# Kernel tuning notes

Measured on AMD Instinct MI355X. Metric: run time of the kernel, lower is better.

The kernel has to match this reference:

```python
import jax, jax.numpy as jnp
import numpy as np

B, D_DATA, D_DICT0, N_SAE, D_DICT = 2048, 768, 128, 128, 32


def _kaiming_uniform(key, shape, fan_in):
    # torch.nn.init.kaiming_uniform_ default: bound = sqrt(6 / fan_in) / sqrt(5-gain stuff) ~ use gain=sqrt(2)? match torch default a=sqrt(5) not needed; plain kaiming_uniform_ uses gain=sqrt(2): bound = sqrt(6/fan_in)*? Keep simple: bound = sqrt(6.0/fan_in)
    bound = np.sqrt(6.0 / fan_in)
    return jax.random.uniform(key, shape, jnp.float32, -bound, bound)


def setup_inputs() -> dict:
    key = jax.random.key(0)
    ks = jax.random.split(key, 6)
    x = jax.random.normal(ks[0], (B, D_DATA), jnp.float32)
    # top-level SAE params
    W_enc0 = _kaiming_uniform(ks[1], (D_DATA, D_DICT0), D_DATA)
    b_enc0 = jnp.zeros((D_DICT0,), jnp.float32)
    W_dec0 = _kaiming_uniform(ks[2], (D_DICT0, D_DATA), D_DICT0)
    W_dec0 = W_dec0 / jnp.linalg.norm(W_dec0, axis=-1, keepdims=True)
    b_dec0 = jnp.zeros((D_DATA,), jnp.float32)
    # sublayer (hierarchical) per-expert params
    W_enc1 = _kaiming_uniform(ks[3], (N_SAE, D_DATA, D_DICT), D_DATA)
    b_enc1 = jnp.zeros((N_SAE, D_DICT), jnp.float32)
    W_dec1 = _kaiming_uniform(ks[4], (N_SAE, D_DICT, D_DATA), D_DICT)
    W_dec1 = W_dec1 / jnp.linalg.norm(W_dec1, axis=-1, keepdims=True)
    b_dec1 = jnp.zeros((N_SAE, D_DATA), jnp.float32)
    return {"x": x, "W_enc0": W_enc0, "b_enc0": b_enc0, "W_dec0": W_dec0,
            "b_dec0": b_dec0, "W_enc1": W_enc1, "b_enc1": b_enc1,
            "W_dec1": W_dec1, "b_dec1": b_dec1}


def reference(x, W_enc0, b_enc0, W_dec0, b_dec0, W_enc1, b_enc1, W_dec1, b_dec1):
    # ---- sae_0 (standard SAE; scale/unscale are identity) ----
    acts0 = jax.nn.relu((x - b_dec0) @ W_enc0 + b_enc0)        # [B, D_DICT0]
    x0 = acts0 @ W_dec0 + b_dec0                               # [B, D_DATA]
    # ---- binary gate over experts (n_sae == d_dict0) ----
    gate = (acts0 > 0).astype(x.dtype)                         # [B, N_SAE]
    # ---- sublayer: gather-encode-decode-scatter, expressed densely with a
    # binary mask (gate only selects membership; gate value is not multiplied).
    # Avoid materializing [B, N_SAE, D_DATA] by distributing (x - b_dec1[j]):
    pre = (jnp.einsum('bd,jdk->bjk', x, W_enc1)
           - jnp.einsum('jd,jdk->jk', b_dec1, W_enc1)[None]
           + b_enc1[None])                                     # [B, N_SAE, D_DICT]
    acts1 = jax.nn.relu(pre) * gate[:, :, None]                # zero out ungated
    # scatter_add over experts: sum_j gated (acts1[b,j] @ W_dec1[j] + b_dec1[j])
    dec = jnp.einsum('bjk,jkd->bd', acts1, W_dec1) + gate @ b_dec1  # [B, D_DATA]
    return x0 + dec
```

## Files before the change

### kernel.cpp

```cpp
#include <hip/hip_runtime.h>
#include <hip/hip_bf16.h>
#include <stdint.h>

#define B_SZ   2048
#define DDATA  768
#define NSAE   128
#define NJK    4096
#define KA2    4352
#define SPLITK 4
#define KC2    1088

typedef unsigned short u16;
typedef short bf16x8 __attribute__((ext_vector_type(8)));
typedef float f32x4  __attribute__((ext_vector_type(4)));

static __device__ __forceinline__ u16 f2bf(float f) {
  __hip_bfloat16 h = __float2bfloat16(f);
  return *reinterpret_cast<u16*>(&h);
}

static __device__ __forceinline__ void gload16(const u16* g, u16* l) {
  __builtin_amdgcn_global_load_lds(
      (const __attribute__((address_space(1))) unsigned int*)g,
      (__attribute__((address_space(3))) unsigned int*)l,
      16, 0, 0);
}

__global__ __launch_bounds__(256) void k_front(const float* __restrict__ x,
                                               const float* __restrict__ We0,
                                               const float* __restrict__ be0,
                                               const float* __restrict__ bd0,
                                               const float* __restrict__ We1,
                                               const float* __restrict__ bd1,
                                               const float* __restrict__ be1,
                                               const float* __restrict__ Wd1,
                                               const float* __restrict__ Wd0,
                                               u16* __restrict__ W1T,
                                               float* __restrict__ cvp,
                                               u16* __restrict__ B2T,
                                               u16* __restrict__ xb,
                                               u16* __restrict__ A2) {
  __shared__ float smem[6280];
  const int bid = blockIdx.x, t = threadIdx.x;
  if (bid < 512) {
    const int b0 = bid * 4;
    float* xs   = smem;
    float* part = smem + 3072;
    float* wqp  = smem + 5120;
    float* xns  = smem + 5632;
#pragma unroll
    for (int i = 0; i < 3; ++i) {
      int idx = t + i * 256;
      int r = idx / 192, c4 = idx % 192;
      size_t go = (size_t)(b0 + r) * DDATA + c4 * 4;
      float4 v = *(const float4*)&x[go];
      ushort4 o;
      o.x = f2bf(v.x); o.y = f2bf(v.y); o.z = f2bf(v.z); o.w = f2bf(v.w);
      *(ushort4*)&xb[go] = o;
      float4 b4 = *(const float4*)&bd0[c4 * 4];
      v.x -= b4.x; v.y -= b4.y; v.z -= b4.z; v.w -= b4.w;
      *(float4*)&xs[r * DDATA + c4 * 4] = v;
    }
    __syncthreads();
    const int ln = t & 63, w = t >> 6;
    {
      float a = 0.f;
#pragma unroll
      for (int q = 0; q < 12; ++q) { float xv = xs[w * DDATA + ln + q * 64]; a += xv * xv; }
#pragma unroll
      for (int sh = 32; sh; sh >>= 1) a += __shfl_xor(a, sh, 64);
      if (ln == 0) xns[w] = a;
    }
    const int j0 = ln * 2;
    float a00=0.f,a01=0.f,a10=0.f,a11=0.f,a20=0.f,a21=0.f,a30=0.f,a31=0.f;
    float wq0=0.f, wq1=0.f;
    const int dbase = w * 192;
    for (int d = dbase; d < dbase + 192; d += 4) {
      float4 xv0 = *(const float4*)&xs[0 * DDATA + d];
      float4 xv1 = *(const float4*)&xs[1 * DDATA + d];
      float4 xv2 = *(const float4*)&xs[2 * DDATA + d];
      float4 xv3 = *(const float4*)&xs[3 * DDATA + d];
#pragma unroll
      for (int dd = 0; dd < 4; ++dd) {
        float2 w2 = *(const float2*)&We0[(size_t)(d + dd) * 128 + j0];
        float x0 = ((const float*)&xv0)[dd], x1 = ((const float*)&xv1)[dd];
        float x2 = ((const float*)&xv2)[dd], x3 = ((const float*)&xv3)[dd];
        a00 += x0 * w2.x; a01 += x0 * w2.y;
        a10 += x1 * w2.x; a11 += x1 * w2.y;
        a20 += x2 * w2.x; a21 += x2 * w2.y;
        a30 += x3 * w2.x; a31 += x3 * w2.y;
        wq0 += w2.x * w2.x; wq1 += w2.y * w2.y;
      }
    }
    *(float2*)&part[(w * 4 + 0) * 128 + j0] = make_float2(a00, a01);
    *(float2*)&part[(w * 4 + 1) * 128 + j0] = make_float2(a10, a11);
    *(float2*)&part[(w * 4 + 2) * 128 + j0] = make_float2(a20, a21);
    *(float2*)&part[(w * 4 + 3) * 128 + j0] = make_float2(a30, a31);
    *(float2*)&wqp[w * 128 + j0] = make_float2(wq0, wq1);
    __syncthreads();
    float p0 = be0[j0], p1 = be0[j0 + 1];
    float wn0 = 0.f, wn1 = 0.f;
#pragma unroll
    for (int q = 0; q < 4; ++q) {
      float2 pr = *(const float2*)&part[(q * 4 + w) * 128 + j0];
      p0 += pr.x; p1 += pr.y;
      float2 wr2 = *(const float2*)&wqp[q * 128 + j0];
      wn0 += wr2.x; wn1 += wr2.y;
    }
    const float sx = sqrtf(xns[w]);
    const float tau0 = 1e-4f * sx * sqrtf(wn0);
    const float tau1 = 1e-4f * sx * sqrtf(wn1);
    const int bb = b0 + w;
    const size_t row = (size_t)bb * KA2;
    unsigned pk = (unsigned)f2bf(p0 > 0.f ? p0 : 0.f) |
                  ((unsigned)f2bf(p1 > 0.f ? p1 : 0.f) << 16);
    unsigned gk = (p0 > 0.f ? 0x3F80u : 0u) | (p1 > 0.f ? 0x3F800000u : 0u);
    *(unsigned*)&A2[row + NJK + j0]       = pk;
    *(unsigned*)&A2[row + NJK + 128 + j0] = gk;
#pragma unroll
    for (int c = 0; c < 2; ++c) {
      float pv = c ? p1 : p0;
      float tv = c ? tau1 : tau0;
      unsigned long long mask = __ballot(fabsf(pv) <= tv);
      while (mask) {
        int src = (int)__builtin_ctzll(mask);
        mask &= mask - 1;
        int jj = src * 2 + c;
        double acc = 0.0;
#pragma unroll
        for (int q = 0; q < 12; ++q) {
          int d = ln + q * 64;
          acc += (double)(x[(size_t)bb * DDATA + d] - bd0[d]) *
                 (double)We0[(size_t)d * 128 + jj];
        }
#pragma unroll
        for (int sh = 32; sh; sh >>= 1) acc += __shfl_xor(acc, sh, 64);
        if (ln == src) {
          double pd = acc + (double)be0[jj];
          A2[row + NJK + jj]       = f2bf(pd > 0.0 ? (float)pd : 0.f);
          A2[row + NJK + 128 + jj] = (pd > 0.0) ? (u16)0x3F80 : (u16)0;
        }
      }
    }
  } else if (bid < 896) {
    const int e = bid - 512;
    const int j = e & 127, seg = e >> 7;
    float* ts  = smem;
    float* bds = smem + 64 * 33;
    float* red = smem + 64 * 33 + 64;
    const int k = t & 31, g = t >> 5;
    float cacc = 0.f;
    for (int db = seg * 4; db < seg * 4 + 4; ++db) {
      const float* src = We1 + (size_t)j * 24576 + db * 2048;
#pragma unroll
      for (int i = 0; i < 8; ++i) {
        int ee = t + i * 256;
        ts[(ee >> 5) * 33 + (ee & 31)] = src[ee];
      }
      if (t < 64) bds[t] = bd1[(size_t)j * DDATA + db * 64 + t];
      __syncthreads();
#pragma unroll
      for (int i = 0; i < 8; ++i) {
        int ee = t + i * 256;
        int kk = ee >> 6, d = ee & 63;
        W1T[(size_t)(j * 32 + kk) * DDATA + db * 64 + d] = f2bf(ts[d * 33 + kk]);
      }
#pragma unroll
      for (int q = 0; q < 8; ++q) {
        int d = g + 8 * q;
        cacc += ts[d * 33 + k] * bds[d];
      }
      __syncthreads();
    }
    red[g * 32 + k] = cacc;
    __syncthreads();
    if (g == 0) {
      float s = 0.f;
#pragma unroll
      for (int q = 0; q < 8; ++q) s += red[q * 32 + k];
      cvp[seg * 4096 + j * 32 + k] = (seg == 0 ? be1[j * 32 + k] : 0.f) - s;
    }
  } else {
    const int e2 = bid - 896;
    const int rb = e2 / 12, dbk = e2 % 12;
    const float* src; int r0, base;
    if (rb < 64)      { src = Wd1; r0 = rb * 64;        base = 0;    }
    else if (rb < 66) { src = Wd0; r0 = (rb - 64) * 64; base = 4096; }
    else              { src = bd1; r0 = (rb - 66) * 64; base = 4224; }
    const int d0 = dbk * 64;
#pragma unroll
    for (int i = 0; i < 16; ++i) {
      int ee = t + i * 256;
      int ri = ee >> 6, di = ee & 63;
      smem[ri * 65 + di] = src[(size_t)(r0 + ri) * DDATA + d0 + di];
    }
    __syncthreads();
#pragma unroll
    for (int i = 0; i < 16; ++i) {
      int ee = t + i * 256;
      int di = ee >> 6, ri = ee & 63;
      B2T[(size_t)(d0 + di) * KA2 + base + r0 + ri] = f2bf(smem[ri * 65 + di]);
    }
  }
}

template<int BM, int BN, int EPI>
__global__ __launch_bounds__(256) void k_gemm(const u16* __restrict__ A,
                                              const u16* __restrict__ Bm,
                                              int K, int Kc,
                                              float* __restrict__ outF,
                                              u16* __restrict__ A2,
                                              const float* __restrict__ cvec) {
  constexpr int WM = BM / 32, WN = BN / 32;
  __shared__ __align__(16) u16 As[BM * 64];
  __shared__ __align__(16) u16 Bs[BN * 64];
  __shared__ u16 gate_s[BM * 4];
  __shared__ float cv_s[BN];
  const int tid = threadIdx.x;
  int bx, by, bz;
  {
    const int h = blockIdx.x;
    if (EPI == 1) {
      const int l = (h & 7) * 64 + (h >> 3);
      const int g2 = l >> 6, w = l & 63;
      by = w >> 2; bx = (g2 << 2) + (w & 3); bz = 0;
    } else {
      const int l = (h & 7) * 96 + (h >> 3);
      bx = l >> 7; const int r2 = l & 127; bz = r2 >> 5; by = r2 & 31;
    }
  }
  const int kbase = bz * Kc;
  const u16* Ab = A  + (size_t)(by * BM) * K;
  const u16* Bb = Bm + (size_t)(bx * BN) * K;
  const int wave = tid >> 6, lane = tid & 63;
  const int wr = wave >> 1, wc = wave & 1;
  const int m0 = wr * (BM / 2), n0 = wc * (BN / 2);
  const int lm = lane & 15, qd = lane >> 4;

  if (EPI == 1) {
    for (int e = tid; e < BM * 4; e += 256) {
      int r = e >> 2, q = e & 3;
      gate_s[e] = A2[(size_t)(by * BM + r) * KA2 + NJK + 128 + bx * 4 + q];
    }
    for (int e = tid; e < BN; e += 256)
      cv_s[e] = cvec[bx * BN + e] + cvec[4096 + bx * BN + e] + cvec[8192 + bx * BN + e];
  }

  f32x4 acc[WM][WN];
  const f32x4 zero = {0.f, 0.f, 0.f, 0.f};
  for (int mi = 0; mi < WM; ++mi)
    for (int ni = 0; ni < WN; ++ni) acc[mi][ni] = zero;

  for (int k0 = kbase; k0 < kbase + Kc; k0 += 64) {
#pragma unroll
    for (int i = 0; i < BM / 32; ++i) {
      int id = tid + 256 * i;
      int row = id >> 3, u = id & 7;
      gload16(Ab + (size_t)row * K + k0 + ((u ^ (row & 7)) * 8), &As[id * 8]);
    }
#pragma unroll
    for (int i = 0; i < BN / 32; ++i) {
      int id = tid + 256 * i;
      int row = id >> 3, u = id & 7;
      gload16(Bb + (size_t)row * K + k0 + ((u ^ (row & 7)) * 8), &Bs[id * 8]);
    }
    __syncthreads();
#pragma unroll
    for (int s = 0; s < 2; ++s) {
      const int swz = ((s << 2) + qd) ^ (lm & 7);
      bf16x8 af[WM], bfv[WN];
#pragma unroll
      for (int mi = 0; mi < WM; ++mi)
        af[mi] = *(const bf16x8*)&As[(m0 + mi * 16 + lm) * 64 + swz * 8];
#pragma unroll
      for (int ni = 0; ni < WN; ++ni)
        bfv[ni] = *(const bf16x8*)&Bs[(n0 + ni * 16 + lm) * 64 + swz * 8];
#pragma unroll
      for (int mi = 0; mi < WM; ++mi)
#pragma unroll
        for (int ni = 0; ni < WN; ++ni)
          acc[mi][ni] = __builtin_amdgcn_mfma_f32_16x16x32_bf16(af[mi], bfv[ni],
                                                                acc[mi][ni], 0, 0, 0);
    }
    __syncthreads();
  }

  const int rb = qd * 4;
#pragma unroll
  for (int mi = 0; mi < WM; ++mi) {
#pragma unroll
    for (int ni = 0; ni < WN; ++ni) {
#pragma unroll
      for (int r = 0; r < 4; ++r) {
        int ml = m0 + mi * 16 + rb + r;
        int nl = n0 + ni * 16 + lm;
        int gm = by * BM + ml;
        int gn = bx * BN + nl;
        float v = acc[mi][ni][r];
        if (EPI == 1) {
          v += cv_s[nl];
          v = v > 0.f ? v : 0.f;
          u16 gbit = gate_s[ml * 4 + (nl >> 5)];
          v = gbit ? v : 0.f;
          float vn = __shfl_xor(v, 1, 64);
          if ((lm & 1) == 0) {
            unsigned pk = (unsigned)f2bf(v) | ((unsigned)f2bf(vn) << 16);
            *(unsigned*)&A2[(size_t)gm * KA2 + gn] = pk;
          }
        } else {
          outF[((size_t)bz * B_SZ + gm) * DDATA + gn] = v;
        }
      }
    }
  }
}

__global__ __launch_bounds__(256) void k_reduce(const float* __restrict__ part,
                                                const float* __restrict__ bias,
                                                float* __restrict__ out) {
  const int N4 = B_SZ * DDATA / 4;
  int i = blockIdx.x * 256 + threadIdx.x;
  const float4* p4 = (const float4*)part;
  float4 s = p4[i];
#pragma unroll
  for (int z = 1; z < SPLITK; ++z) {
    float4 t = p4[i + z * N4];
    s.x += t.x; s.y += t.y; s.z += t.z; s.w += t.w;
  }
  float4 b = ((const float4*)bias)[i % (DDATA / 4)];
  s.x += b.x; s.y += b.y; s.z += b.z; s.w += b.w;
  ((float4*)out)[i] = s;
}

extern "C" void kernel_launch(void* const* d_in, const int* in_sizes, int n_in,
                              void* d_out, int out_size, void* d_ws, size_t ws_size,
                              hipStream_t stream) {
  const float* x   = (const float*)d_in[0];
  const float* We0 = (const float*)d_in[1];
  const float* be0 = (const float*)d_in[2];
  const float* Wd0 = (const float*)d_in[3];
  const float* bd0 = (const float*)d_in[4];
  const float* We1 = (const float*)d_in[5];
  const float* be1 = (const float*)d_in[6];
  const float* Wd1 = (const float*)d_in[7];
  const float* bd1 = (const float*)d_in[8];
  float* out = (float*)d_out;

  uint8_t* ws = (uint8_t*)d_ws;
  size_t off = 0;
  auto carve = [&](size_t bytes) {
    uint8_t* p = ws + off;
    off += (bytes + 255) & ~(size_t)255;
    return p;
  };
  u16*    A2   = (u16*)carve((size_t)B_SZ * KA2 * 2);
  u16*    xb   = (u16*)carve((size_t)B_SZ * DDATA * 2);
  u16*    W1T  = (u16*)carve((size_t)NJK * DDATA * 2);
  u16*    B2T  = (u16*)carve((size_t)DDATA * KA2 * 2);
  float*  cvp  = (float*)carve((size_t)3 * NJK * 4);
  float*  part = (float*)carve((size_t)SPLITK * B_SZ * DDATA * 4);

  k_front <<<1712, 256, 0, stream>>>(x, We0, be0, bd0, We1, bd1, be1, Wd1, Wd0,
                                     W1T, cvp, B2T, xb, A2);
  k_gemm<128, 128, 1><<<512, 256, 0, stream>>>(xb, W1T, DDATA, DDATA,
                                               nullptr, A2, cvp);
  k_gemm<64, 128, 2><<<768, 256, 0, stream>>>(A2, B2T, KA2, KC2,
                                              part, nullptr, nullptr);
  k_reduce<<<1536, 256, 0, stream>>>(part, bd0, out);
}
```

Baseline: 161.6 us.

## Double-buffer LDS tiles in GEMM to overlap global loads with MFMA

Splits the A and B shared-memory tiles into two buffers and issues the async global-to-LDS loads for the next k-tile before computing the current one. Explicit vmcnt waits let the current tile's loads finish while the next tile's remain in flight, and raw s_barrier replaces __syncthreads. This hides global load latency behind MFMA work, at the cost of double LDS usage and possibly lower occupancy. The second barrier is needed so the next iteration's stage does not overwrite a buffer still being read, and the vmcnt values assume a fixed count of loads per stage.

```diff
diff --git a/kernel.cpp b/kernel.cpp
--- a/kernel.cpp
+++ b/kernel.cpp
@@ -212,8 +212,9 @@
                                               u16* __restrict__ A2,
                                               const float* __restrict__ cvec) {
   constexpr int WM = BM / 32, WN = BN / 32;
-  __shared__ __align__(16) u16 As[BM * 64];
-  __shared__ __align__(16) u16 Bs[BN * 64];
+  constexpr int LPS = BM / 32 + BN / 32;
+  __shared__ __align__(16) u16 As[2][BM * 64];
+  __shared__ __align__(16) u16 Bs[2][BN * 64];
   __shared__ u16 gate_s[BM * 4];
   __shared__ float cv_s[BN];
   const int tid = threadIdx.x;
@@ -251,30 +252,45 @@
   for (int mi = 0; mi < WM; ++mi)
     for (int ni = 0; ni < WN; ++ni) acc[mi][ni] = zero;
 
-  for (int k0 = kbase; k0 < kbase + Kc; k0 += 64) {
+  auto stage = [&](int kt, int buf) {
+    const int k0 = kbase + kt * 64;
 #pragma unroll
     for (int i = 0; i < BM / 32; ++i) {
       int id = tid + 256 * i;
       int row = id >> 3, u = id & 7;
-      gload16(Ab + (size_t)row * K + k0 + ((u ^ (row & 7)) * 8), &As[id * 8]);
+      gload16(Ab + (size_t)row * K + k0 + ((u ^ (row & 7)) * 8), &As[buf][id * 8]);
     }
 #pragma unroll
     for (int i = 0; i < BN / 32; ++i) {
       int id = tid + 256 * i;
       int row = id >> 3, u = id & 7;
-      gload16(Bb + (size_t)row * K + k0 + ((u ^ (row & 7)) * 8), &Bs[id * 8]);
-    }
-    __syncthreads();
+      gload16(Bb + (size_t)row * K + k0 + ((u ^ (row & 7)) * 8), &Bs[buf][id * 8]);
+    }
+  };
+
+  const int NT = Kc / 64;
+  stage(0, 0);
+  for (int t = 0; t < NT; ++t) {
+    const int cur = t & 1;
+    if (t + 1 < NT) {
+      stage(t + 1, cur ^ 1);
+      if constexpr (LPS == 8)      asm volatile("s_waitcnt vmcnt(8)" ::: "memory");
+      else if constexpr (LPS == 6) asm volatile("s_waitcnt vmcnt(6)" ::: "memory");
+      else                         asm volatile("s_waitcnt vmcnt(0)" ::: "memory");
+    } else {
+      asm volatile("s_waitcnt vmcnt(0)" ::: "memory");
+    }
+    __builtin_amdgcn_s_barrier();
 #pragma unroll
     for (int s = 0; s < 2; ++s) {
       const int swz = ((s << 2) + qd) ^ (lm & 7);
       bf16x8 af[WM], bfv[WN];
 #pragma unroll
       for (int mi = 0; mi < WM; ++mi)
-        af[mi] = *(const bf16x8*)&As[(m0 + mi * 16 + lm) * 64 + swz * 8];
+        af[mi] = *(const bf16x8*)&As[cur][(m0 + mi * 16 + lm) * 64 + swz * 8];
 #pragma unroll
       for (int ni = 0; ni < WN; ++ni)
-        bfv[ni] = *(const bf16x8*)&Bs[(n0 + ni * 16 + lm) * 64 + swz * 8];
+        bfv[ni] = *(const bf16x8*)&Bs[cur][(n0 + ni * 16 + lm) * 64 + swz * 8];
 #pragma unroll
       for (int mi = 0; mi < WM; ++mi)
 #pragma unroll
@@ -282,7 +298,8 @@
           acc[mi][ni] = __builtin_amdgcn_mfma_f32_16x16x32_bf16(af[mi], bfv[ni],
                                                                 acc[mi][ni], 0, 0, 0);
     }
-    __syncthreads();
+    if (t + 1 < NT)
+      __builtin_amdgcn_s_barrier();
   }
 
   const int rb = qd * 4;
```

Result: faster. 153.2 us (-5.2%).
